# Optimization experiments

Measured on AMD Instinct MI355X. Metric: run time of the kernel, lower is better.

The kernel has to match this reference:

```python
import jax, jax.numpy as jnp
import numpy as np

N = 50000  # nodes
E = 1600000  # directed edges
F_IN = 64
H = 64
C = 16
EPS = 1e-12


def setup_inputs() -> dict:
    key = jax.random.key(0)
    ks = jax.random.split(key, 10)
    x = jax.random.normal(ks[0], (N, F_IN), jnp.float32)
    edge_index = jax.random.randint(ks[1], (2, E), 0, N, dtype=jnp.int32)
    def lin(k, fan_in, fan_out):
        return jax.random.normal(k, (fan_in, fan_out), jnp.float32) * (1.0 / np.sqrt(fan_in))
    return {
        "x": x,
        "edge_index": edge_index,
        "W1": lin(ks[2], F_IN, H), "b1": jnp.zeros((H,), jnp.float32),
        "W2": lin(ks[3], H, H),    "b2": jnp.zeros((H,), jnp.float32),
        "W3": lin(ks[4], H, H),    "b3": jnp.zeros((H,), jnp.float32),
        "Wlin": lin(ks[5], 3 * H, C), "blin": jnp.zeros((C,), jnp.float32),
    }


def _gcn_norm(edge_index, n):
    # add self loops, compute symmetric GCN normalization D^-1/2 (A+I) D^-1/2
    loop = jnp.arange(n, dtype=edge_index.dtype)
    row = jnp.concatenate([edge_index[0], loop])  # target nodes
    col = jnp.concatenate([edge_index[1], loop])  # source nodes
    deg = jax.ops.segment_sum(jnp.ones_like(row, dtype=jnp.float32), row, num_segments=n)
    dis = jnp.where(deg > 0, jax.lax.rsqrt(jnp.maximum(deg, 1.0)), 0.0)
    norm = dis[row] * dis[col]  # [E+N]
    return row, col, norm


def _gcn_layer(x, row, col, norm, W, b):
    h = x @ W                              # [N, H]
    msg = h[col] * norm[:, None]           # gather sources, scale
    agg = jax.ops.segment_sum(msg, row, num_segments=x.shape[0])  # scatter-add
    return agg + b


def _l2norm(x):
    # torch F.normalize(p=2, dim=1)
    n = jnp.sqrt(jnp.sum(x * x, axis=1, keepdims=True))
    return x / jnp.maximum(n, EPS)


def reference(x, edge_index, W1, b1, W2, b2, W3, b3, Wlin, blin):
    row, col, norm = _gcn_norm(edge_index, x.shape[0])
    stack = []
    h = x
    for (W, b) in ((W1, b1), (W2, b2), (W3, b3)):
        h = _gcn_layer(h, row, col, norm, W, b)
        h = jax.nn.relu(h)
        h = _l2norm(h)
        stack.append(h)
    emb = jnp.concatenate(stack, axis=1)   # [N, 3H]
    out = emb @ Wlin + blin                # [N, C]
    return jax.nn.log_softmax(out, axis=1)
```

## Files before the change

kernel.cpp:

```cpp
#include <hip/hip_runtime.h>
#include <hip/hip_bf16.h>

#define NN 50000
#define NPAD 50048
#define EE 1600000
#define NB 391
#define CAPB 4608
#define CPAD 16
#define EPB 4096
#define BCAP 29
#define PBCAP 7424

typedef __attribute__((ext_vector_type(8))) short short8;
typedef __attribute__((ext_vector_type(4))) float floatx4;

__device__ __forceinline__ float ldext(const void* p, long i, int f32) {
    return f32 ? ((const float*)p)[i]
               : __bfloat162float(((const __hip_bfloat16*)p)[i]);
}

__device__ __forceinline__ unsigned short f2b(float f) {
    __hip_bfloat16 h = __float2bfloat16(f);
    unsigned short u; __builtin_memcpy(&u, &h, 2); return u;
}
__device__ __forceinline__ float asf(unsigned int x) {
    float f; __builtin_memcpy(&f, &x, 4); return f;
}

__global__ void k_bucket(const int* __restrict__ row, const int* __restrict__ col,
                         int* __restrict__ bcur, unsigned int* __restrict__ bdata,
                         const unsigned short* __restrict__ xu, int* __restrict__ flag) {
    __shared__ int lcnt[NB];
    __shared__ unsigned binned[NB * BCAP];
    __shared__ int dcnt;
    int tid = threadIdx.x;
    if (blockIdx.x == 0) {
        if (tid == 0) dcnt = 0;
        __syncthreads();
        int local = 0;
        for (int j = 0; j < 16; ++j) {
            unsigned short u = xu[2 * (tid + 256 * j)];
            int ex = (u >> 7) & 0xFF;
            if (ex == 0xFF || ex < 0x60) local++;
        }
        atomicAdd(&dcnt, local);
        __syncthreads();
        if (tid == 0) flag[0] = (dcnt > 256) ? 1 : 0;
    }
    long base = (long)blockIdx.x * EPB;
    int nedge = (int)min((long)EPB, (long)EE - base);
    for (int k = tid; k < NB; k += 256) lcnt[k] = 0;
    __syncthreads();
    const int4* r4 = (const int4*)(row + base);
    const int4* c4 = (const int4*)(col + base);
    for (int j = tid; j < (nedge >> 2); j += 256) {
        int4 rr = r4[j], cc = c4[j];
        #pragma unroll
        for (int t = 0; t < 4; ++t) {
            int r = (&rr.x)[t], c = (&cc.x)[t];
            int b = r >> 7;
            unsigned rec = ((unsigned)(r & 127) << 16) | (unsigned)c;
            int p = atomicAdd(&lcnt[b], 1);
            if (p < BCAP) binned[b * BCAP + p] = rec;
            else {
                int gp = atomicAdd(&bcur[b * CPAD], 1);
                if (gp < CAPB) bdata[(long)b * CAPB + gp] = rec;
            }
        }
    }
    __syncthreads();
    for (int b = tid; b < NB; b += 256) {
        int n = min(lcnt[b], BCAP);
        if (!n) continue;
        int gb = atomicAdd(&bcur[b * CPAD], n);
        long dst = (long)b * CAPB;
        for (int j = 0; j < n; ++j)
            if (gb + j < CAPB) bdata[dst + gb + j] = binned[b * BCAP + j];
    }
}

__global__ void k_csr(const int* __restrict__ bcur, const unsigned* __restrict__ bdata,
                      int* __restrict__ rp0, int* __restrict__ degA,
                      float* __restrict__ dis, unsigned short* __restrict__ csr_col) {
    __shared__ unsigned recs[CAPB];
    __shared__ int cnt[128];
    __shared__ int incl[128];
    __shared__ int curs[128];
    int b = blockIdx.x, tid = threadIdx.x;
    int lane = tid & 63, wid = tid >> 6;
    if (tid < 128) cnt[tid] = 0;
    __syncthreads();
    int n = min(bcur[b * CPAD], CAPB);
    const unsigned* dp = bdata + (long)b * CAPB;
    for (int i = tid; i < n; i += 256) {
        unsigned rec = dp[i];
        recs[i] = rec;
        atomicAdd(&cnt[(rec >> 16) & 127], 1);
    }
    __syncthreads();
    if (tid < 128) {
        int x = (cnt[tid] + 31) & ~31;
        #pragma unroll
        for (int off = 1; off < 64; off <<= 1) {
            int y = __shfl_up(x, off);
            if (lane >= off) x += y;
        }
        incl[tid] = x;
    }
    __syncthreads();
    int r0 = b << 7;
    int lim = (b + 1) * PBCAP;
    if (tid < 128) {
        int c = cnt[tid];
        int x = (c + 31) & ~31;
        int ic = incl[tid] + (wid == 1 ? incl[63] : 0);
        int excl = b * PBCAP + ic - x;
        curs[tid] = excl;
        int r = r0 + tid;
        if (r < NN) {
            rp0[r] = excl;
            degA[r] = c;
            dis[r] = rsqrtf((float)(c + 1));
        }
        for (int j = c; j < x && excl + j < lim; ++j)
            csr_col[excl + j] = (unsigned short)NN;
    }
    __syncthreads();
    for (int i = tid; i < n; i += 256) {
        unsigned rec = recs[i];
        int p = atomicAdd(&curs[(rec >> 16) & 127], 1);
        if (p < lim) csr_col[p] = (unsigned short)(rec & 0xFFFF);
    }
}

template <bool EXT>
__global__ void k_gemm(const void* __restrict__ X, const void* __restrict__ W,
                       const int* __restrict__ flag, const float* __restrict__ dis,
                       unsigned short* __restrict__ Hout) {
    __shared__ __align__(16) unsigned short xs[64 * 72];
    __shared__ __align__(16) unsigned short wt[64 * 72];
    int tid = threadIdx.x;
    int n0 = blockIdx.x * 64;
    const int f32 = flag[0];
    const unsigned short* Wb = (const unsigned short*)W;
    const float* Wf = (const float*)W;
    if (EXT && f32) {
        for (int idx = tid; idx < 1024; idx += 256) {
            int nn = idx >> 4, sg = idx & 15;
            int n = n0 + nn;
            float4 v = {0.f, 0.f, 0.f, 0.f};
            if (n < NN) v = *(const float4*)((const float*)X + (long)n * 64 + sg * 4);
            ushort4 s;
            s.x = f2b(v.x); s.y = f2b(v.y); s.z = f2b(v.z); s.w = f2b(v.w);
            *(ushort4*)(xs + nn * 72 + sg * 4) = s;
        }
    } else {
        for (int idx = tid; idx < 512; idx += 256) {
            int nn = idx >> 3, sg = idx & 7;
            int n = n0 + nn;
            short8 v = {0, 0, 0, 0, 0, 0, 0, 0};
            if (n < NN) v = *(const short8*)((const unsigned short*)X + (long)n * 64 + sg * 8);
            *(short8*)(xs + nn * 72 + sg * 8) = v;
        }
    }
    if (f32) {
        for (int idx = tid; idx < 1024; idx += 256) {
            int k = idx >> 4, sg = idx & 15;
            float4 v = *(const float4*)(Wf + k * 64 + sg * 4);
            wt[(sg * 4 + 0) * 72 + k] = f2b(v.x);
            wt[(sg * 4 + 1) * 72 + k] = f2b(v.y);
            wt[(sg * 4 + 2) * 72 + k] = f2b(v.z);
            wt[(sg * 4 + 3) * 72 + k] = f2b(v.w);
        }
    } else {
        for (int idx = tid; idx < 512; idx += 256) {
            int k = idx >> 3, sg = idx & 7;
            short8 v = *(const short8*)(Wb + k * 64 + sg * 8);
            #pragma unroll
            for (int j = 0; j < 8; ++j)
                wt[(sg * 8 + j) * 72 + k] = (unsigned short)v[j];
        }
    }
    __syncthreads();
    int lane = tid & 63, wid = tid >> 6;
    int m0 = wid * 16;
    int quad = lane >> 4, nl = lane & 15;
    short8 a0 = *(const short8*)(xs + (m0 + nl) * 72 + quad * 8);
    short8 a1 = *(const short8*)(xs + (m0 + nl) * 72 + quad * 8 + 32);
    floatx4 acc[4];
    #pragma unroll
    for (int ct = 0; ct < 4; ++ct) {
        int n = ct * 16 + nl;
        short8 b0 = *(const short8*)(wt + n * 72 + quad * 8);
        short8 b1 = *(const short8*)(wt + n * 72 + quad * 8 + 32);
        floatx4 c = {0.f, 0.f, 0.f, 0.f};
        c = __builtin_amdgcn_mfma_f32_16x16x32_bf16(a0, b0, c, 0, 0, 0);
        c = __builtin_amdgcn_mfma_f32_16x16x32_bf16(a1, b1, c, 0, 0, 0);
        acc[ct] = c;
    }
    #pragma unroll
    for (int r = 0; r < 4; ++r) {
        int node = n0 + m0 + quad * 4 + r;
        if (node < NN) {
            float dn = dis[node];
            #pragma unroll
            for (int ct = 0; ct < 4; ++ct)
                Hout[(long)node * 64 + ct * 16 + nl] = f2b(dn * acc[ct][r]);
        } else {
            #pragma unroll
            for (int ct = 0; ct < 4; ++ct)
                Hout[(long)node * 64 + ct * 16 + nl] = 0;
        }
    }
}

__global__ void k_agg(const uint4* __restrict__ hp128, const int* __restrict__ rp0,
                      const int* __restrict__ degA, const float* __restrict__ dis,
                      const unsigned short* __restrict__ csr_col,
                      const void* __restrict__ bias, const int* __restrict__ flag,
                      unsigned short* __restrict__ eo ) {
    int lane = threadIdx.x & 63, wid = threadIdx.x >> 6;
    int half = lane >> 5;
    int i = blockIdx.x * 8 + wid * 2 + half;
    bool valid = (i < NN);
    int iv = valid ? i : 0;
    int q4 = (lane >> 3) & 3;
    int fl = lane & 7;
    float2 A0 = {0,0}, A1 = {0,0}, A2 = {0,0}, A3 = {0,0};
    #define ADDU(u) do { \
        A0.x += asf((u).x << 16); A0.y += asf((u).x & 0xFFFF0000u); \
        A1.x += asf((u).y << 16); A1.y += asf((u).y & 0xFFFF0000u); \
        A2.x += asf((u).z << 16); A2.y += asf((u).z & 0xFFFF0000u); \
        A3.x += asf((u).w << 16); A3.y += asf((u).w & 0xFFFF0000u); } while (0)
    if (valid && q4 == 0) {
        uint4 u = hp128[(long)iv * 8 + fl];
        ADDU(u);
    }
    int e0 = rp0[iv];
    int pd = (degA[iv] + 31) & ~31;
    const unsigned short* cb = csr_col + e0 + q4 * 8;
    for (int t = 0; t < pd; t += 32) {
        uint4 I = *(const uint4*)(cb + t);
        int c0 = (int)(I.x & 0xFFFFu), c1 = (int)(I.x >> 16);
        int c2 = (int)(I.y & 0xFFFFu), c3 = (int)(I.y >> 16);
        int c4 = (int)(I.z & 0xFFFFu), c5 = (int)(I.z >> 16);
        int c6 = (int)(I.w & 0xFFFFu), c7 = (int)(I.w >> 16);
        uint4 u0 = hp128[(long)c0 * 8 + fl];
        uint4 u1 = hp128[(long)c1 * 8 + fl];
        uint4 u2 = hp128[(long)c2 * 8 + fl];
        uint4 u3 = hp128[(long)c3 * 8 + fl];
        uint4 u4 = hp128[(long)c4 * 8 + fl];
        uint4 u5 = hp128[(long)c5 * 8 + fl];
        uint4 u6 = hp128[(long)c6 * 8 + fl];
        uint4 u7 = hp128[(long)c7 * 8 + fl];
        ADDU(u0); ADDU(u1); ADDU(u2); ADDU(u3);
        ADDU(u4); ADDU(u5); ADDU(u6); ADDU(u7);
    }
    #undef ADDU
    #pragma unroll
    for (int off = 8; off < 32; off <<= 1) {
        A0.x += __shfl_xor(A0.x, off); A0.y += __shfl_xor(A0.y, off);
        A1.x += __shfl_xor(A1.x, off); A1.y += __shfl_xor(A1.y, off);
        A2.x += __shfl_xor(A2.x, off); A2.y += __shfl_xor(A2.y, off);
        A3.x += __shfl_xor(A3.x, off); A3.y += __shfl_xor(A3.y, off);
    }
    const int f32 = flag[0];
    float di = dis[iv];
    float v0 = fmaf(di, A0.x, ldext(bias, 8 * fl + 0, f32));
    float v1 = fmaf(di, A0.y, ldext(bias, 8 * fl + 1, f32));
    float v2 = fmaf(di, A1.x, ldext(bias, 8 * fl + 2, f32));
    float v3 = fmaf(di, A1.y, ldext(bias, 8 * fl + 3, f32));
    float v4 = fmaf(di, A2.x, ldext(bias, 8 * fl + 4, f32));
    float v5 = fmaf(di, A2.y, ldext(bias, 8 * fl + 5, f32));
    float v6 = fmaf(di, A3.x, ldext(bias, 8 * fl + 6, f32));
    float v7 = fmaf(di, A3.y, ldext(bias, 8 * fl + 7, f32));
    v0 = fmaxf(v0, 0.f); v1 = fmaxf(v1, 0.f); v2 = fmaxf(v2, 0.f); v3 = fmaxf(v3, 0.f);
    v4 = fmaxf(v4, 0.f); v5 = fmaxf(v5, 0.f); v6 = fmaxf(v6, 0.f); v7 = fmaxf(v7, 0.f);
    float s = fmaf(v0, v0, fmaf(v1, v1, fmaf(v2, v2, v3 * v3)))
            + fmaf(v4, v4, fmaf(v5, v5, fmaf(v6, v6, v7 * v7)));
    #pragma unroll
    for (int off = 4; off; off >>= 1) s += __shfl_xor(s, off);
    float inv = 1.f / fmaxf(sqrtf(s), 1e-12f);
    if (valid && q4 == 0) {
        union { unsigned short us[8]; uint4 v; } pk;
        pk.us[0] = f2b(v0 * inv); pk.us[1] = f2b(v1 * inv);
        pk.us[2] = f2b(v2 * inv); pk.us[3] = f2b(v3 * inv);
        pk.us[4] = f2b(v4 * inv); pk.us[5] = f2b(v5 * inv);
        pk.us[6] = f2b(v6 * inv); pk.us[7] = f2b(v7 * inv);
        *(uint4*)(eo + (long)i * 64 + 8 * fl) = pk.v;
    }
}

__global__ void k_out(const unsigned short* __restrict__ emb, const void* __restrict__ Wlin,
                      const void* __restrict__ blin, const int* __restrict__ flag,
                      void* __restrict__ out) {
    int tid = threadIdx.x, lane = tid & 63, wid = tid >> 6;
    int quad = lane >> 4, nl = lane & 15;
    int base = blockIdx.x * 64 + wid * 16;
    const int f32 = flag[0];
    const unsigned short* Wb = (const unsigned short*)Wlin;
    const float* Wf = (const float*)Wlin;
    int ia = min(base + nl, NN - 1);
    floatx4 c = {0.f, 0.f, 0.f, 0.f};
    #pragma unroll
    for (int kc = 0; kc < 6; ++kc) {
        short8 b;
        #pragma unroll
        for (int j = 0; j < 8; ++j) {
            int k = kc * 32 + quad * 8 + j;
            b[j] = (short)(f32 ? f2b(Wf[k * 16 + nl]) : Wb[k * 16 + nl]);
        }
        int L = kc >> 1, ko = (kc & 1) * 32 + quad * 8;
        short8 a = *(const short8*)(emb + (long)L * NN * 64 + (long)ia * 64 + ko);
        c = __builtin_amdgcn_mfma_f32_16x16x32_bf16(a, b, c, 0, 0, 0);
    }
    float bl = ldext(blin, nl, f32);
    #pragma unroll
    for (int r = 0; r < 4; ++r) {
        float v = c[r] + bl;
        float m = v;
        #pragma unroll
        for (int off = 1; off < 16; off <<= 1) m = fmaxf(m, __shfl_xor(m, off));
        float ex = __expf(v - m);
        float s = ex;
        #pragma unroll
        for (int off = 1; off < 16; off <<= 1) s += __shfl_xor(s, off);
        float o = (v - m) - __logf(s);
        int node = base + quad * 4 + r;
        if (node < NN) {
            long oidx = (long)node * 16 + nl;
            if (f32) ((float*)out)[oidx] = o;
            else     ((__hip_bfloat16*)out)[oidx] = __float2bfloat16(o);
        }
    }
}

extern "C" void kernel_launch(void* const* d_in, const int* in_sizes, int n_in,
                              void* d_out, int out_size, void* d_ws, size_t ws_size,
                              hipStream_t stream) {
    const void* x    = d_in[0];
    const int*  ei   = (const int*)d_in[1];
    const void* W1   = d_in[2];
    const void* b1   = d_in[3];
    const void* W2   = d_in[4];
    const void* b2   = d_in[5];
    const void* W3   = d_in[6];
    const void* b3   = d_in[7];
    const void* Wlin = d_in[8];
    const void* blin = d_in[9];

    unsigned short* h   = (unsigned short*)d_ws;
    unsigned short* emb = h + (long)NPAD * 64;
    float* dis     = (float*)(emb + (long)3 * NN * 64);
    int*   rp0     = (int*)(dis + NN);
    int*   degA    = rp0 + NN;
    int*   flag    = degA + NN;
    int*   bcur    = flag + 16;
    unsigned* bdata = (unsigned*)(bcur + NB * CPAD);
    unsigned short* csr_col = (unsigned short*)(bdata + (long)NB * CAPB);

    const int* row = ei;
    const int* col = ei + EE;

    (void)hipMemsetAsync(bcur, 0, NB * CPAD * sizeof(int), stream);
    k_bucket<<<(EE + EPB - 1) / EPB, 256, 0, stream>>>(row, col, bcur, bdata,
                                                       (const unsigned short*)x, flag);
    k_csr<<<NB, 256, 0, stream>>>(bcur, bdata, rp0, degA, dis, csr_col);

    int gb = (NN + 63) / 64;
    int ga = (NN + 7) / 8;
    const uint4* hp128 = (const uint4*)h;
    k_gemm<true><<<gb, 256, 0, stream>>>(x, W1, flag, dis, h);
    k_agg<<<ga, 256, 0, stream>>>(hp128, rp0, degA, dis, csr_col, b1, flag, emb);
    k_gemm<false><<<gb, 256, 0, stream>>>(emb, W2, flag, dis, h);
    k_agg<<<ga, 256, 0, stream>>>(hp128, rp0, degA, dis, csr_col, b2, flag,
                                  emb + (long)NN * 64);
    k_gemm<false><<<gb, 256, 0, stream>>>(emb + (long)NN * 64, W3, flag, dis, h);
    k_agg<<<ga, 256, 0, stream>>>(hp128, rp0, degA, dis, csr_col, b3, flag,
                                  emb + (long)2 * NN * 64);

    k_out<<<gb, 256, 0, stream>>>(emb, Wlin, blin, flag, d_out);
}
```

Before: 259.7 us.

## Fuse output head and log-softmax into last aggregation kernel

```diff
diff --git a/kernel.cpp b/kernel.cpp
--- a/kernel.cpp
+++ b/kernel.cpp
@@ -24,6 +24,10 @@
     unsigned short u; __builtin_memcpy(&u, &h, 2); return u;
 }
 __device__ __forceinline__ float asf(unsigned int x) {
+    float f; __builtin_memcpy(&f, &x, 4); return f;
+}
+__device__ __forceinline__ float b2f(unsigned short u) {
+    unsigned int x = ((unsigned int)u) << 16;
     float f; __builtin_memcpy(&f, &x, 4); return f;
 }
 
@@ -206,7 +210,7 @@
             #pragma unroll
             for (int ct = 0; ct < 4; ++ct)
                 Hout[(long)node * 64 + ct * 16 + nl] = f2b(dn * acc[ct][r]);
-        } else {
+        } else if (EXT) {
             #pragma unroll
             for (int ct = 0; ct < 4; ++ct)
                 Hout[(long)node * 64 + ct * 16 + nl] = 0;
@@ -214,11 +218,15 @@
     }
 }
 
+template <bool HEAD>
 __global__ void k_agg(const uint4* __restrict__ hp128, const int* __restrict__ rp0,
                       const int* __restrict__ degA, const float* __restrict__ dis,
                       const unsigned short* __restrict__ csr_col,
                       const void* __restrict__ bias, const int* __restrict__ flag,
-                      unsigned short* __restrict__ eo ) {
+                      unsigned short* __restrict__ eo ,
+                      const unsigned short* __restrict__ embp ,
+                      const void* __restrict__ Wlin, const void* __restrict__ blin,
+                      void* __restrict__ outp) {
     int lane = threadIdx.x & 63, wid = threadIdx.x >> 6;
     int half = lane >> 5;
     int i = blockIdx.x * 8 + wid * 2 + half;
@@ -281,56 +289,85 @@
     #pragma unroll
     for (int off = 4; off; off >>= 1) s += __shfl_xor(s, off);
     float inv = 1.f / fmaxf(sqrtf(s), 1e-12f);
-    if (valid && q4 == 0) {
-        union { unsigned short us[8]; uint4 v; } pk;
-        pk.us[0] = f2b(v0 * inv); pk.us[1] = f2b(v1 * inv);
-        pk.us[2] = f2b(v2 * inv); pk.us[3] = f2b(v3 * inv);
-        pk.us[4] = f2b(v4 * inv); pk.us[5] = f2b(v5 * inv);
-        pk.us[6] = f2b(v6 * inv); pk.us[7] = f2b(v7 * inv);
-        *(uint4*)(eo + (long)i * 64 + 8 * fl) = pk.v;
-    }
-}
-
-__global__ void k_out(const unsigned short* __restrict__ emb, const void* __restrict__ Wlin,
-                      const void* __restrict__ blin, const int* __restrict__ flag,
-                      void* __restrict__ out) {
-    int tid = threadIdx.x, lane = tid & 63, wid = tid >> 6;
-    int quad = lane >> 4, nl = lane & 15;
-    int base = blockIdx.x * 64 + wid * 16;
-    const int f32 = flag[0];
-    const unsigned short* Wb = (const unsigned short*)Wlin;
-    const float* Wf = (const float*)Wlin;
-    int ia = min(base + nl, NN - 1);
-    floatx4 c = {0.f, 0.f, 0.f, 0.f};
-    #pragma unroll
-    for (int kc = 0; kc < 6; ++kc) {
-        short8 b;
+    if (!HEAD) {
+        if (valid && q4 == 0) {
+            union { unsigned short us[8]; uint4 v; } pk;
+            pk.us[0] = f2b(v0 * inv); pk.us[1] = f2b(v1 * inv);
+            pk.us[2] = f2b(v2 * inv); pk.us[3] = f2b(v3 * inv);
+            pk.us[4] = f2b(v4 * inv); pk.us[5] = f2b(v5 * inv);
+            pk.us[6] = f2b(v6 * inv); pk.us[7] = f2b(v7 * inv);
+            *(uint4*)(eo + (long)i * 64 + 8 * fl) = pk.v;
+        }
+    } else {
+        float e2[8] = {v0 * inv, v1 * inv, v2 * inv, v3 * inv,
+                       v4 * inv, v5 * inv, v6 * inv, v7 * inv};
+        uint4 uL0 = *(const uint4*)(embp + (long)iv * 64 + 8 * fl);
+        uint4 uL1 = *(const uint4*)(embp + (long)NN * 64 + (long)iv * 64 + 8 * fl);
+        float eA[8], eB[8];
+        {
+            const unsigned* w0 = &uL0.x;
+            const unsigned* w1 = &uL1.x;
+            #pragma unroll
+            for (int j = 0; j < 4; ++j) {
+                eA[2 * j]     = asf(w0[j] << 16);
+                eA[2 * j + 1] = asf(w0[j] & 0xFFFF0000u);
+                eB[2 * j]     = asf(w1[j] << 16);
+                eB[2 * j + 1] = asf(w1[j] & 0xFFFF0000u);
+            }
+        }
+        const float* Wf = (const float*)Wlin;
+        const unsigned short* Wb = (const unsigned short*)Wlin;
+        int cb4 = q4 * 4;
+        float p0 = 0.f, p1 = 0.f, p2 = 0.f, p3 = 0.f;
         #pragma unroll
         for (int j = 0; j < 8; ++j) {
-            int k = kc * 32 + quad * 8 + j;
-            b[j] = (short)(f32 ? f2b(Wf[k * 16 + nl]) : Wb[k * 16 + nl]);
-        }
-        int L = kc >> 1, ko = (kc & 1) * 32 + quad * 8;
-        short8 a = *(const short8*)(emb + (long)L * NN * 64 + (long)ia * 64 + ko);
-        c = __builtin_amdgcn_mfma_f32_16x16x32_bf16(a, b, c, 0, 0, 0);
-    }
-    float bl = ldext(blin, nl, f32);
-    #pragma unroll
-    for (int r = 0; r < 4; ++r) {
-        float v = c[r] + bl;
-        float m = v;
+            int k0 = 8 * fl + j;
+            float4 wv0, wv1, wv2;
+            if (f32) {
+                wv0 = *(const float4*)(Wf + k0 * 16 + cb4);
+                wv1 = *(const float4*)(Wf + (k0 + 64) * 16 + cb4);
+                wv2 = *(const float4*)(Wf + (k0 + 128) * 16 + cb4);
+            } else {
+                ushort4 a = *(const ushort4*)(Wb + k0 * 16 + cb4);
+                ushort4 b = *(const ushort4*)(Wb + (k0 + 64) * 16 + cb4);
+                ushort4 c = *(const ushort4*)(Wb + (k0 + 128) * 16 + cb4);
+                wv0 = {b2f(a.x), b2f(a.y), b2f(a.z), b2f(a.w)};
+                wv1 = {b2f(b.x), b2f(b.y), b2f(b.z), b2f(b.w)};
+                wv2 = {b2f(c.x), b2f(c.y), b2f(c.z), b2f(c.w)};
+            }
+            p0 = fmaf(eA[j], wv0.x, fmaf(eB[j], wv1.x, fmaf(e2[j], wv2.x, p0)));
+            p1 = fmaf(eA[j], wv0.y, fmaf(eB[j], wv1.y, fmaf(e2[j], wv2.y, p1)));
+            p2 = fmaf(eA[j], wv0.z, fmaf(eB[j], wv1.z, fmaf(e2[j], wv2.z, p2)));
+            p3 = fmaf(eA[j], wv0.w, fmaf(eB[j], wv1.w, fmaf(e2[j], wv2.w, p3)));
+        }
         #pragma unroll
-        for (int off = 1; off < 16; off <<= 1) m = fmaxf(m, __shfl_xor(m, off));
-        float ex = __expf(v - m);
-        float s = ex;
-        #pragma unroll
-        for (int off = 1; off < 16; off <<= 1) s += __shfl_xor(s, off);
-        float o = (v - m) - __logf(s);
-        int node = base + quad * 4 + r;
-        if (node < NN) {
-            long oidx = (long)node * 16 + nl;
-            if (f32) ((float*)out)[oidx] = o;
-            else     ((__hip_bfloat16*)out)[oidx] = __float2bfloat16(o);
+        for (int off = 1; off < 8; off <<= 1) {
+            p0 += __shfl_xor(p0, off);
+            p1 += __shfl_xor(p1, off);
+            p2 += __shfl_xor(p2, off);
+            p3 += __shfl_xor(p3, off);
+        }
+        p0 += ldext(blin, cb4 + 0, f32);
+        p1 += ldext(blin, cb4 + 1, f32);
+        p2 += ldext(blin, cb4 + 2, f32);
+        p3 += ldext(blin, cb4 + 3, f32);
+        float m = fmaxf(fmaxf(p0, p1), fmaxf(p2, p3));
+        m = fmaxf(m, __shfl_xor(m, 8));
+        m = fmaxf(m, __shfl_xor(m, 16));
+        float es = __expf(p0 - m) + __expf(p1 - m) + __expf(p2 - m) + __expf(p3 - m);
+        es += __shfl_xor(es, 8);
+        es += __shfl_xor(es, 16);
+        float lg = __logf(es);
+        if (valid && fl == 0) {
+            float o0 = (p0 - m) - lg, o1 = (p1 - m) - lg;
+            float o2 = (p2 - m) - lg, o3 = (p3 - m) - lg;
+            if (f32) {
+                float4 ov = {o0, o1, o2, o3};
+                *(float4*)((float*)outp + (long)i * 16 + cb4) = ov;
+            } else {
+                ushort4 ov = {f2b(o0), f2b(o1), f2b(o2), f2b(o3)};
+                *(ushort4*)((__hip_bfloat16*)outp + (long)i * 16 + cb4) = ov;
+            }
         }
     }
 }
@@ -371,13 +408,13 @@
     int ga = (NN + 7) / 8;
     const uint4* hp128 = (const uint4*)h;
     k_gemm<true><<<gb, 256, 0, stream>>>(x, W1, flag, dis, h);
-    k_agg<<<ga, 256, 0, stream>>>(hp128, rp0, degA, dis, csr_col, b1, flag, emb);
+    k_agg<false><<<ga, 256, 0, stream>>>(hp128, rp0, degA, dis, csr_col, b1, flag,
+                                         emb, nullptr, nullptr, nullptr, nullptr);
     k_gemm<false><<<gb, 256, 0, stream>>>(emb, W2, flag, dis, h);
-    k_agg<<<ga, 256, 0, stream>>>(hp128, rp0, degA, dis, csr_col, b2, flag,
-                                  emb + (long)NN * 64);
+    k_agg<false><<<ga, 256, 0, stream>>>(hp128, rp0, degA, dis, csr_col, b2, flag,
+                                         emb + (long)NN * 64, nullptr, nullptr,
+                                         nullptr, nullptr);
     k_gemm<false><<<gb, 256, 0, stream>>>(emb + (long)NN * 64, W3, flag, dis, h);
-    k_agg<<<ga, 256, 0, stream>>>(hp128, rp0, degA, dis, csr_col, b3, flag,
-                                  emb + (long)2 * NN * 64);
-
-    k_out<<<gb, 256, 0, stream>>>(emb, Wlin, blin, flag, d_out);
-}
+    k_agg<true><<<ga, 256, 0, stream>>>(hp128, rp0, degA, dis, csr_col, b3, flag,
+                                        nullptr, emb, Wlin, blin, d_out);
+}
```

After: 311.8 us. 1.2x slower.
